# Kernel tuning notes

Hardware: AMD Instinct MI355X
Metric: run time of the kernel (lower is better)

## Reference

```python
import jax, jax.numpy as jnp
import numpy as np

B, U, D, N, O = 128, 16, 256, 1024, 256
RES_CONN, IN_CONN, BIAS_P = 0.2, 0.2, 0.5


def _fixed_bernoulli(rng, heads, rows, cols, conn):
    # each column has exactly nb = int(conn*rows) ones (as in the torch code)
    nb = max(1, int(conn * rows))
    r = rng.random((heads, rows, cols))
    thr = np.sort(r, axis=1)[:, nb - 1:nb, :]
    return (r <= thr).astype(np.float32)


def setup_inputs() -> dict:
    rng = np.random.default_rng(0)
    # recurrent weights: normal * fixed-bernoulli mask, normalized by spectral radius
    W = rng.normal(size=(U, N, N)).astype(np.float32) * _fixed_bernoulli(rng, U, N, N, RES_CONN)
    sr0 = np.abs(np.linalg.eigvals(W.astype(np.float64))).max(axis=-1).astype(np.float32).reshape(U, 1, 1)
    W = W / sr0
    Win = _fixed_bernoulli(rng, U, D, N, IN_CONN)
    bias = (rng.random((U, 1, N)) < BIAS_P).astype(np.float32)
    Wout = rng.normal(size=(U, N, O)).astype(np.float32)
    adaptive_lr = rng.random((U, D, 1)).astype(np.float32)
    sr = rng.random((U, 1, 1)).astype(np.float32)
    temperature = np.ones((1,), np.float32)
    X = rng.normal(size=(B, U, D)).astype(np.float32)
    state = rng.normal(size=(B, U, N)).astype(np.float32)
    arrs = dict(X=X, state=state, W=W, Win=Win, bias=bias, Wout=Wout,
                sr=sr, adaptive_lr=adaptive_lr, temperature=temperature)
    return {k: jnp.asarray(v) for k, v in arrs.items()}


def reference(X, state, W, Win, bias, Wout, sr, adaptive_lr, temperature):
    # X: [B,U,D] -> [B,U,1,D]; state: [B,U,N] -> [B,U,1,N]
    x = X[:, :, None, :]
    s = state[:, :, None, :]
    # adaptive per-unit learning rate: softmax over the units axis
    lr = jax.nn.softmax(jnp.einsum('buid,udk->buik', x, adaptive_lr) / temperature, axis=1)  # [B,U,1,1]
    feed = jnp.einsum('buid,udn->buin', x, Win)            # [B,U,1,N]
    echo = jnp.einsum('buin,unm->buim', s, W * sr) + bias  # [B,U,1,N]
    new_state = (1.0 - lr) * s + lr * jnp.tanh(feed + echo)
    output = jnp.einsum('buin,uno->buio', new_state, Wout)  # [B,U,1,O]
    return new_state[:, :, 0, :], output[:, :, 0, :]
```

## Files before the change

### kernel.cpp

```cpp
#include <hip/hip_runtime.h>
#include <math.h>

#define Bsz 128
#define Usz 16
#define Dsz 256
#define Nsz 1024
#define Osz 256
#define BK  64

typedef __attribute__((ext_vector_type(2))) unsigned int u32x2;
typedef __attribute__((ext_vector_type(4))) unsigned int u32x4;
typedef __attribute__((ext_vector_type(4))) float f32x4;
typedef __attribute__((ext_vector_type(8))) short bf16x8;

union cell_u { u32x4 u; bf16x8 b; };
union cell2_u { u32x2 u; };

__device__ __forceinline__ unsigned int fbits(float f) {
    union { float f; unsigned int u; } v; v.f = f; return v.u;
}
__device__ __forceinline__ unsigned int pk(float lo, float hi) {
    return __builtin_amdgcn_perm(fbits(hi), fbits(lo), 0x07060302u);
}
__device__ __forceinline__ u32x2 pk4(f32x4 v, float s) {
    v *= s;
    u32x2 r; r[0] = pk(v[0], v[1]); r[1] = pk(v[2], v[3]);
    return r;
}
__device__ __forceinline__ bf16x8 ldB8(const float* p, size_t str) {
    const float x0 = p[0],       x1 = p[str],     x2 = p[2*str], x3 = p[3*str];
    const float x4 = p[4*str],   x5 = p[5*str],   x6 = p[6*str], x7 = p[7*str];
    cell_u r;
    r.u[0] = pk(x0, x1); r.u[1] = pk(x2, x3);
    r.u[2] = pk(x4, x5); r.u[3] = pk(x6, x7);
    return r.b;
}

__global__ __launch_bounds__(256)
void lr_kernel(const float* __restrict__ X, const float* __restrict__ alr,
               const float* __restrict__ temp, float* __restrict__ lr)
{
    const int b = blockIdx.x;
    const int t = threadIdx.x;
    const int u = t >> 4;
    const int l = t & 15;
    const float* xp = X + ((size_t)b * Usz + u) * Dsz;
    const float* ap = alr + (size_t)u * Dsz;
    float s = 0.f;
    for (int d = l; d < Dsz; d += 16) s += xp[d] * ap[d];
    s += __shfl_down(s, 8, 16);
    s += __shfl_down(s, 4, 16);
    s += __shfl_down(s, 2, 16);
    s += __shfl_down(s, 1, 16);
    __shared__ float logits[16];
    if (l == 0) logits[u] = s;
    __syncthreads();
    if (t < 16) {
        const float T = temp[0];
        float m = -1e30f;
        #pragma unroll
        for (int i = 0; i < 16; i++) m = fmaxf(m, logits[i] / T);
        float sum = 0.f;
        #pragma unroll
        for (int i = 0; i < 16; i++) sum += expf(logits[i] / T - m);
        lr[(size_t)b * Usz + t] = expf(logits[t] / T - m) / sum;
    }
}

__global__ __launch_bounds__(256)
void state_gemm(const float* __restrict__ X, const float* __restrict__ state,
                const float* __restrict__ W, const float* __restrict__ Win,
                const float* __restrict__ bias, const float* __restrict__ sr,
                const float* __restrict__ lr, float* __restrict__ out0)
{
    const int id = blockIdx.x;
    const int u  = id & 15;
    const int nt = id >> 4;

    const int tid  = threadIdx.x;
    const int wave = tid >> 6, lane = tid & 63;
    const int l16  = lane & 15, kgl = lane >> 4;
    const int wm = wave & 1, wn = wave >> 1;

    __shared__ unsigned short As[2][128 * 72];

    const float sru = sr[u];

    const int r0 = tid >> 4;
    const int c  = tid & 15;

    f32x4 ra[8];

    auto ldA = [&](int s) {
        const int k0 = s * BK;
        if (k0 < Dsz) {
            const float* base = X + ((size_t)r0 * Usz + u) * Dsz + k0 + c * 4;
            #pragma unroll
            for (int i = 0; i < 8; i++)
                ra[i] = *(const f32x4*)(base + (size_t)16 * i * Usz * Dsz);
        } else {
            const float* base = state + ((size_t)r0 * Usz + u) * Nsz + (k0 - Dsz) + c * 4;
            #pragma unroll
            for (int i = 0; i < 8; i++)
                ra[i] = *(const f32x4*)(base + (size_t)16 * i * Usz * Nsz);
        }
    };
    auto wrA = [&](int p, float sc) {
        #pragma unroll
        for (int i = 0; i < 8; i++)
            *(u32x2*)&As[p][(r0 + 16 * i) * 72 + c * 4] = pk4(ra[i], sc);
    };

    f32x4 acc[4][2] = {};

    auto comp = [&](int s, int p) {
        const int k0 = s * BK;
        const float* bbase = (k0 < Dsz)
            ? Win + (size_t)u * Dsz * Nsz + (size_t)k0 * Nsz
            : W   + (size_t)u * Nsz * Nsz + (size_t)(k0 - Dsz) * Nsz;
        const int col = nt * 64 + wn * 32 + l16;
        #pragma unroll
        for (int kk = 0; kk < 2; kk++) {
            const float* bp = bbase + (size_t)(kk * 32 + kgl * 8) * Nsz + col;
            const bf16x8 bf0 = ldB8(bp, Nsz);
            const bf16x8 bf1 = ldB8(bp + 16, Nsz);
            #pragma unroll
            for (int mi = 0; mi < 4; mi++) {
                const bf16x8 af = *(const bf16x8*)&As[p][(wm * 64 + mi * 16 + l16) * 72 + kk * 32 + kgl * 8];
                acc[mi][0] = __builtin_amdgcn_mfma_f32_16x16x32_bf16(af, bf0, acc[mi][0], 0, 0, 0);
                acc[mi][1] = __builtin_amdgcn_mfma_f32_16x16x32_bf16(af, bf1, acc[mi][1], 0, 0, 0);
            }
        }
    };

    ldA(0); wrA(0, 1.f);
    ldA(1);
    __syncthreads();
    for (int s = 0; s < 20; s++) {
        const int p = s & 1;
        if (s + 1 < 20) wrA(p ^ 1, (s + 1 < 4) ? 1.f : sru);
        if (s + 2 < 20) ldA(s + 2);
        comp(s, p);
        __syncthreads();
    }

    #pragma unroll
    for (int ni = 0; ni < 2; ni++) {
        const int gcol = nt * 64 + wn * 32 + ni * 16 + l16;
        const float bi = bias[u * Nsz + gcol];
        #pragma unroll
        for (int mi = 0; mi < 4; mi++) {
            #pragma unroll
            for (int rg = 0; rg < 4; rg++) {
                const int grow = wm * 64 + mi * 16 + kgl * 4 + rg;
                const size_t idx = ((size_t)grow * Usz + u) * Nsz + gcol;
                const float th = tanhf(acc[mi][ni][rg] + bi);
                const float lv = lr[grow * Usz + u];
                out0[idx] = (1.f - lv) * state[idx] + lv * th;
            }
        }
    }
}

__global__ __launch_bounds__(256)
void out_gemm(const float* __restrict__ ns, const float* __restrict__ Wout,
              float* __restrict__ dst, int nsteps, int partial)
{
    const int id = blockIdx.x;
    const int u  = id & 15;
    const int ot = (id >> 4) & 3;
    const int ks = id >> 6;
    const int kbase = ks * nsteps * BK;

    const int tid  = threadIdx.x;
    const int wave = tid >> 6, lane = tid & 63;
    const int l16  = lane & 15, kgl = lane >> 4;
    const int wm = wave & 1, wn = wave >> 1;

    __shared__ unsigned short As[2][128 * 72];

    const int r0 = tid >> 4;
    const int c  = tid & 15;

    f32x4 ra[8];
    auto ldA = [&](int s) {
        const float* base = ns + ((size_t)r0 * Usz + u) * Nsz + kbase + s * BK + c * 4;
        #pragma unroll
        for (int i = 0; i < 8; i++)
            ra[i] = *(const f32x4*)(base + (size_t)16 * i * Usz * Nsz);
    };
    auto wrA = [&](int p) {
        #pragma unroll
        for (int i = 0; i < 8; i++)
            *(u32x2*)&As[p][(r0 + 16 * i) * 72 + c * 4] = pk4(ra[i], 1.f);
    };

    f32x4 acc[4][2] = {};
    auto comp = [&](int s, int p) {
        const float* bbase = Wout + (size_t)u * Nsz * Osz + (size_t)(kbase + s * BK) * Osz;
        const int col = ot * 64 + wn * 32 + l16;
        #pragma unroll
        for (int kk = 0; kk < 2; kk++) {
            const float* bp = bbase + (size_t)(kk * 32 + kgl * 8) * Osz + col;
            const bf16x8 bf0 = ldB8(bp, Osz);
            const bf16x8 bf1 = ldB8(bp + 16, Osz);
            #pragma unroll
            for (int mi = 0; mi < 4; mi++) {
                const bf16x8 af = *(const bf16x8*)&As[p][(wm * 64 + mi * 16 + l16) * 72 + kk * 32 + kgl * 8];
                acc[mi][0] = __builtin_amdgcn_mfma_f32_16x16x32_bf16(af, bf0, acc[mi][0], 0, 0, 0);
                acc[mi][1] = __builtin_amdgcn_mfma_f32_16x16x32_bf16(af, bf1, acc[mi][1], 0, 0, 0);
            }
        }
    };

    ldA(0); wrA(0);
    if (nsteps > 1) ldA(1);
    __syncthreads();
    for (int s = 0; s < nsteps; s++) {
        const int p = s & 1;
        if (s + 1 < nsteps) wrA(p ^ 1);
        if (s + 2 < nsteps) ldA(s + 2);
        comp(s, p);
        __syncthreads();
    }

    #pragma unroll
    for (int ni = 0; ni < 2; ni++) {
        const int gcol = ot * 64 + wn * 32 + ni * 16 + l16;
        #pragma unroll
        for (int mi = 0; mi < 4; mi++) {
            #pragma unroll
            for (int rg = 0; rg < 4; rg++) {
                const int grow = wm * 64 + mi * 16 + kgl * 4 + rg;
                if (partial)
                    dst[(((size_t)ks * 16 + u) * 128 + grow) * 256 + gcol] = acc[mi][ni][rg];
                else
                    dst[((size_t)grow * Usz + u) * Osz + gcol] = acc[mi][ni][rg];
            }
        }
    }
}

__global__ __launch_bounds__(256)
void out_reduce(const float* __restrict__ part, float* __restrict__ out1)
{
    const size_t i = (size_t)blockIdx.x * 256 + threadIdx.x;
    const size_t base = i * 4;
    const int m = (int)(base >> 12);
    const int u = (int)((base >> 8) & 15);
    const int o = (int)(base & 255);

    const size_t pb = ((size_t)u * 128 + m) * 256 + o;
    const size_t slab = (size_t)16 * 128 * 256;
    f32x4 s = *(const f32x4*)(part + pb);
    s += *(const f32x4*)(part + pb + slab);
    s += *(const f32x4*)(part + pb + 2 * slab);
    s += *(const f32x4*)(part + pb + 3 * slab);
    *(f32x4*)(out1 + base) = s;
}

extern "C" void kernel_launch(void* const* d_in, const int* in_sizes, int n_in,
                              void* d_out, int out_size, void* d_ws, size_t ws_size,
                              hipStream_t stream)
{
    (void)in_sizes; (void)n_in; (void)out_size;
    const float* X     = (const float*)d_in[0];
    const float* state = (const float*)d_in[1];
    const float* W     = (const float*)d_in[2];
    const float* Win   = (const float*)d_in[3];
    const float* bias  = (const float*)d_in[4];
    const float* Wout  = (const float*)d_in[5];
    const float* sr    = (const float*)d_in[6];
    const float* alr   = (const float*)d_in[7];
    const float* temp  = (const float*)d_in[8];

    float* out0 = (float*)d_out;
    float* out1 = out0 + (size_t)Bsz * Usz * Nsz;
    float* lr   = (float*)d_ws;

    const size_t p_off   = 8192;
    const size_t p_bytes = (size_t)4 * 16 * 128 * 256 * 4;

    lr_kernel<<<Bsz, 256, 0, stream>>>(X, alr, temp, lr);
    state_gemm<<<256, 256, 0, stream>>>(X, state, W, Win, bias, sr, lr, out0);

    if (ws_size >= p_off + p_bytes) {
        float* part = (float*)((char*)d_ws + p_off);
        out_gemm<<<256, 256, 0, stream>>>(out0, Wout, part, 4, 1);
        out_reduce<<<512, 256, 0, stream>>>(part, out1);
    } else {
        out_gemm<<<64, 256, 0, stream>>>(out0, Wout, out1, 16, 0);
    }
}
```

Measured before the change: 193.7 us.

## Stage B tiles in per-wave LDS and stream A fragments from global

Both GEMM kernels now load the weight operand with vectorized float4 global loads. They convert it to bf16 and transpose it into a swizzled, wave-private LDS buffer, replacing the old strided scalar B loads. The A operand is read directly from global into MFMA fragments instead of being staged in shared LDS. Blocks shrink to two waves with a 32-column tile, the grid doubles, and the block barriers are dropped. The trade-off is that each wave reloads the same B tile and A reads are repeated across column tiles, which leans on L2. The lr kernel dot product is also vectorized.

```diff
diff --git a/kernel.cpp b/kernel.cpp
--- a/kernel.cpp
+++ b/kernel.cpp
@@ -7,6 +7,7 @@
 #define Nsz 1024
 #define Osz 256
 #define BK  64
+#define LDT 72
 
 typedef __attribute__((ext_vector_type(2))) unsigned int u32x2;
 typedef __attribute__((ext_vector_type(4))) unsigned int u32x4;
@@ -14,7 +15,6 @@
 typedef __attribute__((ext_vector_type(8))) short bf16x8;
 
 union cell_u { u32x4 u; bf16x8 b; };
-union cell2_u { u32x2 u; };
 
 __device__ __forceinline__ unsigned int fbits(float f) {
     union { float f; unsigned int u; } v; v.f = f; return v.u;
@@ -22,18 +22,8 @@
 __device__ __forceinline__ unsigned int pk(float lo, float hi) {
     return __builtin_amdgcn_perm(fbits(hi), fbits(lo), 0x07060302u);
 }
-__device__ __forceinline__ u32x2 pk4(f32x4 v, float s) {
-    v *= s;
-    u32x2 r; r[0] = pk(v[0], v[1]); r[1] = pk(v[2], v[3]);
-    return r;
-}
-__device__ __forceinline__ bf16x8 ldB8(const float* p, size_t str) {
-    const float x0 = p[0],       x1 = p[str],     x2 = p[2*str], x3 = p[3*str];
-    const float x4 = p[4*str],   x5 = p[5*str],   x6 = p[6*str], x7 = p[7*str];
-    cell_u r;
-    r.u[0] = pk(x0, x1); r.u[1] = pk(x2, x3);
-    r.u[2] = pk(x4, x5); r.u[3] = pk(x6, x7);
-    return r.b;
+__device__ __forceinline__ unsigned short bf16t(float f) {
+    return (unsigned short)(fbits(f) >> 16);
 }
 
 __global__ __launch_bounds__(256)
@@ -44,10 +34,14 @@
     const int t = threadIdx.x;
     const int u = t >> 4;
     const int l = t & 15;
-    const float* xp = X + ((size_t)b * Usz + u) * Dsz;
-    const float* ap = alr + (size_t)u * Dsz;
+    const f32x4* xp = (const f32x4*)(X + ((size_t)b * Usz + u) * Dsz + l * 16);
+    const f32x4* ap = (const f32x4*)(alr + (size_t)u * Dsz + l * 16);
     float s = 0.f;
-    for (int d = l; d < Dsz; d += 16) s += xp[d] * ap[d];
+    #pragma unroll
+    for (int j = 0; j < 4; j++) {
+        const f32x4 xv = xp[j], av = ap[j];
+        s += xv[0]*av[0] + xv[1]*av[1] + xv[2]*av[2] + xv[3]*av[3];
+    }
     s += __shfl_down(s, 8, 16);
     s += __shfl_down(s, 4, 16);
     s += __shfl_down(s, 2, 16);
@@ -67,92 +61,109 @@
     }
 }
 
-__global__ __launch_bounds__(256)
+__global__ __launch_bounds__(128)
 void state_gemm(const float* __restrict__ X, const float* __restrict__ state,
                 const float* __restrict__ W, const float* __restrict__ Win,
                 const float* __restrict__ bias, const float* __restrict__ sr,
                 const float* __restrict__ lr, float* __restrict__ out0)
 {
     const int id = blockIdx.x;
-    const int u  = id & 15;
-    const int nt = id >> 4;
+    const int nt = id & 31;
+    const int u  = id >> 5;
 
     const int tid  = threadIdx.x;
-    const int wave = tid >> 6, lane = tid & 63;
+    const int wv   = tid >> 6;
+    const int lane = tid & 63;
     const int l16  = lane & 15, kgl = lane >> 4;
-    const int wm = wave & 1, wn = wave >> 1;
-
-    __shared__ unsigned short As[2][128 * 72];
+    const int kL   = lane >> 3;
+    const int c    = lane & 7;
+    const int nB   = 4 * c;
+    const int col0 = nt * 32;
+    const int m0   = wv * 64;
+
+    __shared__ unsigned short Bs[2][2][32 * LDT];
 
     const float sru = sr[u];
 
-    const int r0 = tid >> 4;
-    const int c  = tid & 15;
-
-    f32x4 ra[8];
-
-    auto ldA = [&](int s) {
-        const int k0 = s * BK;
-        if (k0 < Dsz) {
-            const float* base = X + ((size_t)r0 * Usz + u) * Dsz + k0 + c * 4;
-            #pragma unroll
-            for (int i = 0; i < 8; i++)
-                ra[i] = *(const f32x4*)(base + (size_t)16 * i * Usz * Dsz);
-        } else {
-            const float* base = state + ((size_t)r0 * Usz + u) * Nsz + (k0 - Dsz) + c * 4;
-            #pragma unroll
-            for (int i = 0; i < 8; i++)
-                ra[i] = *(const f32x4*)(base + (size_t)16 * i * Usz * Nsz);
-        }
-    };
-    auto wrA = [&](int p, float sc) {
-        #pragma unroll
-        for (int i = 0; i < 8; i++)
-            *(u32x2*)&As[p][(r0 + 16 * i) * 72 + c * 4] = pk4(ra[i], sc);
-    };
-
-    f32x4 acc[4][2] = {};
-
-    auto comp = [&](int s, int p) {
+    f32x4 rbE[8], rbO[8];
+
+    auto ldB = [&](int s, f32x4 (&rb)[8]) {
         const int k0 = s * BK;
         const float* bbase = (k0 < Dsz)
-            ? Win + (size_t)u * Dsz * Nsz + (size_t)k0 * Nsz
-            : W   + (size_t)u * Nsz * Nsz + (size_t)(k0 - Dsz) * Nsz;
-        const int col = nt * 64 + wn * 32 + l16;
+            ? Win + (size_t)u * Dsz * Nsz + (size_t)(k0 + kL) * Nsz + col0 + nB
+            : W   + (size_t)u * Nsz * Nsz + (size_t)(k0 - Dsz + kL) * Nsz + col0 + nB;
+        #pragma unroll
+        for (int j = 0; j < 8; j++)
+            rb[j] = *(const f32x4*)(bbase + (size_t)8 * j * Nsz);
+    };
+    auto wrB = [&](int p, f32x4 (&rb)[8], float sc) {
+        unsigned short* bs = &Bs[wv][p][0];
+        #pragma unroll
+        for (int j = 0; j < 8; j++) {
+            const int go = ((j ^ c) << 3) + kL;
+            #pragma unroll
+            for (int e = 0; e < 4; e++)
+                bs[(nB + e) * LDT + go] = bf16t(rb[j][e] * sc);
+        }
+    };
+    auto rdB = [&](int p, int ni, int kk) -> bf16x8 {
+        const int n = ni * 16 + l16;
+        const int go = ((kk * 4 + kgl) ^ (n >> 2)) << 3;
+        return *(const bf16x8*)&Bs[wv][p][n * LDT + go];
+    };
+    auto ldAf = [&](int s, int mi, int kk) -> bf16x8 {
+        const int k = s * BK + kk * 32 + kgl * 8;
+        const int r = m0 + mi * 16 + l16;
+        const float* ap = (k < Dsz)
+            ? X     + ((size_t)r * Usz + u) * Dsz + k
+            : state + ((size_t)r * Usz + u) * Nsz + (k - Dsz);
+        const f32x4 a0 = *(const f32x4*)ap;
+        const f32x4 a1 = *(const f32x4*)(ap + 4);
+        cell_u af;
+        af.u[0] = pk(a0[0], a0[1]); af.u[1] = pk(a0[2], a0[3]);
+        af.u[2] = pk(a1[0], a1[1]); af.u[3] = pk(a1[2], a1[3]);
+        return af.b;
+    };
+
+    f32x4 acc[4][2] = {};
+    auto comp = [&](int s, int p) {
         #pragma unroll
         for (int kk = 0; kk < 2; kk++) {
-            const float* bp = bbase + (size_t)(kk * 32 + kgl * 8) * Nsz + col;
-            const bf16x8 bf0 = ldB8(bp, Nsz);
-            const bf16x8 bf1 = ldB8(bp + 16, Nsz);
+            const bf16x8 bf0 = rdB(p, 0, kk);
+            const bf16x8 bf1 = rdB(p, 1, kk);
             #pragma unroll
             for (int mi = 0; mi < 4; mi++) {
-                const bf16x8 af = *(const bf16x8*)&As[p][(wm * 64 + mi * 16 + l16) * 72 + kk * 32 + kgl * 8];
+                const bf16x8 af = ldAf(s, mi, kk);
                 acc[mi][0] = __builtin_amdgcn_mfma_f32_16x16x32_bf16(af, bf0, acc[mi][0], 0, 0, 0);
                 acc[mi][1] = __builtin_amdgcn_mfma_f32_16x16x32_bf16(af, bf1, acc[mi][1], 0, 0, 0);
             }
         }
     };
-
-    ldA(0); wrA(0, 1.f);
-    ldA(1);
-    __syncthreads();
-    for (int s = 0; s < 20; s++) {
-        const int p = s & 1;
-        if (s + 1 < 20) wrA(p ^ 1, (s + 1 < 4) ? 1.f : sru);
-        if (s + 2 < 20) ldA(s + 2);
-        comp(s, p);
-        __syncthreads();
+    auto scB = [&](int s) -> float { return (s * BK < Dsz) ? 1.f : sru; };
+
+    ldB(0, rbE);
+    ldB(1, rbO);
+    wrB(0, rbE, scB(0));
+
+    for (int s2 = 0; s2 < 10; s2++) {
+        const int s = 2 * s2;
+        if (s + 2 < 20) ldB(s + 2, rbE);
+        wrB(1, rbO, scB(s + 1));
+        comp(s, 0);
+        if (s + 3 < 20) ldB(s + 3, rbO);
+        if (s + 2 < 20) wrB(0, rbE, scB(s + 2));
+        comp(s + 1, 1);
     }
 
     #pragma unroll
     for (int ni = 0; ni < 2; ni++) {
-        const int gcol = nt * 64 + wn * 32 + ni * 16 + l16;
+        const int gcol = col0 + ni * 16 + l16;
         const float bi = bias[u * Nsz + gcol];
         #pragma unroll
         for (int mi = 0; mi < 4; mi++) {
             #pragma unroll
             for (int rg = 0; rg < 4; rg++) {
-                const int grow = wm * 64 + mi * 16 + kgl * 4 + rg;
+                const int grow = m0 + mi * 16 + kgl * 4 + rg;
                 const size_t idx = ((size_t)grow * Usz + u) * Nsz + gcol;
                 const float th = tanhf(acc[mi][ni][rg] + bi);
                 const float lv = lr[grow * Usz + u];
@@ -162,76 +173,101 @@
     }
 }
 
-__global__ __launch_bounds__(256)
+__global__ __launch_bounds__(128)
 void out_gemm(const float* __restrict__ ns, const float* __restrict__ Wout,
               float* __restrict__ dst, int nsteps, int partial)
 {
     const int id = blockIdx.x;
-    const int u  = id & 15;
-    const int ot = (id >> 4) & 3;
-    const int ks = id >> 6;
+    const int ot = id & 7;
+    const int u  = (id >> 3) & 15;
+    const int ks = id >> 7;
     const int kbase = ks * nsteps * BK;
 
     const int tid  = threadIdx.x;
-    const int wave = tid >> 6, lane = tid & 63;
+    const int wv   = tid >> 6;
+    const int lane = tid & 63;
     const int l16  = lane & 15, kgl = lane >> 4;
-    const int wm = wave & 1, wn = wave >> 1;
-
-    __shared__ unsigned short As[2][128 * 72];
-
-    const int r0 = tid >> 4;
-    const int c  = tid & 15;
-
-    f32x4 ra[8];
-    auto ldA = [&](int s) {
-        const float* base = ns + ((size_t)r0 * Usz + u) * Nsz + kbase + s * BK + c * 4;
-        #pragma unroll
-        for (int i = 0; i < 8; i++)
-            ra[i] = *(const f32x4*)(base + (size_t)16 * i * Usz * Nsz);
-    };
-    auto wrA = [&](int p) {
-        #pragma unroll
-        for (int i = 0; i < 8; i++)
-            *(u32x2*)&As[p][(r0 + 16 * i) * 72 + c * 4] = pk4(ra[i], 1.f);
+    const int kL   = lane >> 3;
+    const int c    = lane & 7;
+    const int nB   = 4 * c;
+    const int col0 = ot * 32;
+    const int m0   = wv * 64;
+
+    __shared__ unsigned short Bs[2][2][32 * LDT];
+
+    f32x4 rbE[8], rbO[8];
+
+    auto ldB = [&](int s, f32x4 (&rb)[8]) {
+        const float* bbase = Wout + (size_t)u * Nsz * Osz
+                           + (size_t)(kbase + s * BK + kL) * Osz + col0 + nB;
+        #pragma unroll
+        for (int j = 0; j < 8; j++)
+            rb[j] = *(const f32x4*)(bbase + (size_t)8 * j * Osz);
+    };
+    auto wrB = [&](int p, f32x4 (&rb)[8]) {
+        unsigned short* bs = &Bs[wv][p][0];
+        #pragma unroll
+        for (int j = 0; j < 8; j++) {
+            const int go = ((j ^ c) << 3) + kL;
+            #pragma unroll
+            for (int e = 0; e < 4; e++)
+                bs[(nB + e) * LDT + go] = bf16t(rb[j][e]);
+        }
+    };
+    auto rdB = [&](int p, int ni, int kk) -> bf16x8 {
+        const int n = ni * 16 + l16;
+        const int go = ((kk * 4 + kgl) ^ (n >> 2)) << 3;
+        return *(const bf16x8*)&Bs[wv][p][n * LDT + go];
+    };
+    auto ldAf = [&](int s, int mi, int kk) -> bf16x8 {
+        const int k = kbase + s * BK + kk * 32 + kgl * 8;
+        const int r = m0 + mi * 16 + l16;
+        const float* ap = ns + ((size_t)r * Usz + u) * Nsz + k;
+        const f32x4 a0 = *(const f32x4*)ap;
+        const f32x4 a1 = *(const f32x4*)(ap + 4);
+        cell_u af;
+        af.u[0] = pk(a0[0], a0[1]); af.u[1] = pk(a0[2], a0[3]);
+        af.u[2] = pk(a1[0], a1[1]); af.u[3] = pk(a1[2], a1[3]);
+        return af.b;
     };
 
     f32x4 acc[4][2] = {};
     auto comp = [&](int s, int p) {
-        const float* bbase = Wout + (size_t)u * Nsz * Osz + (size_t)(kbase + s * BK) * Osz;
-        const int col = ot * 64 + wn * 32 + l16;
         #pragma unroll
         for (int kk = 0; kk < 2; kk++) {
-            const float* bp = bbase + (size_t)(kk * 32 + kgl * 8) * Osz + col;
-            const bf16x8 bf0 = ldB8(bp, Osz);
-            const bf16x8 bf1 = ldB8(bp + 16, Osz);
+            const bf16x8 bf0 = rdB(p, 0, kk);
+            const bf16x8 bf1 = rdB(p, 1, kk);
             #pragma unroll
             for (int mi = 0; mi < 4; mi++) {
-                const bf16x8 af = *(const bf16x8*)&As[p][(wm * 64 + mi * 16 + l16) * 72 + kk * 32 + kgl * 8];
+                const bf16x8 af = ldAf(s, mi, kk);
                 acc[mi][0] = __builtin_amdgcn_mfma_f32_16x16x32_bf16(af, bf0, acc[mi][0], 0, 0, 0);
                 acc[mi][1] = __builtin_amdgcn_mfma_f32_16x16x32_bf16(af, bf1, acc[mi][1], 0, 0, 0);
             }
         }
     };
 
-    ldA(0); wrA(0);
-    if (nsteps > 1) ldA(1);
-    __syncthreads();
-    for (int s = 0; s < nsteps; s++) {
-        const int p = s & 1;
-        if (s + 1 < nsteps) wrA(p ^ 1);
-        if (s + 2 < nsteps) ldA(s + 2);
-        comp(s, p);
-        __syncthreads();
+    ldB(0, rbE);
+    ldB(1, rbO);
+    wrB(0, rbE);
+
+    for (int s2 = 0; s2 < nsteps / 2; s2++) {
+        const int s = 2 * s2;
+        if (s + 2 < nsteps) ldB(s + 2, rbE);
+        wrB(1, rbO);
+        comp(s, 0);
+        if (s + 3 < nsteps) ldB(s + 3, rbO);
+        if (s + 2 < nsteps) wrB(0, rbE);
+        comp(s + 1, 1);
     }
 
     #pragma unroll
     for (int ni = 0; ni < 2; ni++) {
-        const int gcol = ot * 64 + wn * 32 + ni * 16 + l16;
+        const int gcol = col0 + ni * 16 + l16;
         #pragma unroll
         for (int mi = 0; mi < 4; mi++) {
             #pragma unroll
             for (int rg = 0; rg < 4; rg++) {
-                const int grow = wm * 64 + mi * 16 + kgl * 4 + rg;
+                const int grow = m0 + mi * 16 + kgl * 4 + rg;
                 if (partial)
                     dst[(((size_t)ks * 16 + u) * 128 + grow) * 256 + gcol] = acc[mi][ni][rg];
                 else
@@ -282,13 +318,13 @@
     const size_t p_bytes = (size_t)4 * 16 * 128 * 256 * 4;
 
     lr_kernel<<<Bsz, 256, 0, stream>>>(X, alr, temp, lr);
-    state_gemm<<<256, 256, 0, stream>>>(X, state, W, Win, bias, sr, lr, out0);
+    state_gemm<<<512, 128, 0, stream>>>(X, state, W, Win, bias, sr, lr, out0);
 
     if (ws_size >= p_off + p_bytes) {
         float* part = (float*)((char*)d_ws + p_off);
-        out_gemm<<<256, 256, 0, stream>>>(out0, Wout, part, 4, 1);
+        out_gemm<<<512, 128, 0, stream>>>(out0, Wout, part, 4, 1);
         out_reduce<<<512, 256, 0, stream>>>(part, out1);
     } else {
-        out_gemm<<<64, 256, 0, stream>>>(out0, Wout, out1, 16, 0);
-    }
-}
+        out_gemm<<<128, 128, 0, stream>>>(out0, Wout, out1, 16, 0);
+    }
+}
```

New measurement: 226.2 us. +16.8%, slower.
